# Kernel optimization log

Hardware: AMD Instinct MI355X
Metric: run time of the kernel (lower is better)

Reference implementation:

```python
import jax, jax.numpy as jnp
import numpy as np

N = 50000       # nodes
E = 800000      # edges (avg degree 16)
IN_DIM = 128
EDGE_DIM = 32
OUT_DIM = 128


def setup_inputs() -> dict:
    key = jax.random.key(0)
    ks = jax.random.split(key, 7)
    nfeat = jax.random.normal(ks[0], (N, IN_DIM), jnp.float32)
    etype = jax.random.normal(ks[1], (E, EDGE_DIM), jnp.float32)
    src = jax.random.randint(ks[2], (E,), 0, N)
    dst = jax.random.randint(ks[3], (E,), 0, N)
    scaled = lambda k, shape, fan: jax.random.normal(k, shape, jnp.float32) / np.sqrt(fan).astype(np.float32)
    W_edge = scaled(ks[4], (OUT_DIM, EDGE_DIM), EDGE_DIM)          # edge_map.weight
    W_ne = scaled(ks[5], (OUT_DIM, IN_DIM + OUT_DIM), IN_DIM + OUT_DIM)  # fc_neigh_edge.weight
    b_ne = jnp.zeros((OUT_DIM,), jnp.float32)
    W_self = scaled(ks[6], (OUT_DIM, IN_DIM), IN_DIM)              # fc_self.weight
    b_self = jnp.zeros((OUT_DIM,), jnp.float32)
    eps = jnp.zeros((1,), jnp.float32)                             # init_eps = 0, not learned
    return dict(nfeat=nfeat, etype=etype, src=src, dst=dst,
                W_edge=W_edge, W_ne=W_ne, b_ne=b_ne,
                W_self=W_self, b_self=b_self, eps=eps)


def reference(nfeat, etype, src, dst, W_edge, W_ne, b_ne, W_self, b_self, eps):
    # per-edge message: relu(fc_neigh_edge(cat(src_h, edge_map(etype))))
    # split W_ne to avoid materializing the concatenated [E, in+out] tensor
    W1 = W_ne[:, :IN_DIM]    # acts on src node features
    W2 = W_ne[:, IN_DIM:]    # acts on mapped edge features
    eh = etype @ W_edge.T                              # [E, out]
    src_h = nfeat[src]                                 # gather [E, in]
    m = jax.nn.relu(src_h @ W1.T + eh @ W2.T + b_ne)   # [E, out]
    # max-reduce messages to destination nodes (DGL max reducer; 0 for isolated nodes)
    neigh = jax.ops.segment_max(m, dst, num_segments=N)
    deg = jax.ops.segment_sum(jnp.ones((E,), m.dtype), dst, num_segments=N)
    neigh = jnp.where((deg > 0)[:, None], neigh, jnp.zeros((), m.dtype))
    out = (1.0 + eps) * neigh + (nfeat @ W_self.T + b_self)
    return out
```

## Files before the change

kernel.cpp:

```cpp
#include <hip/hip_runtime.h>
#include <hip/hip_bf16.h>

#define NNODES 50000
#define NEDGES 800000
#define IN_DIM 128
#define EDGE_DIM 32
#define OUT_DIM 128
#define KDIM 160
#define A_STRIDE 168
#define NS 136
#define MT_STRIDE 72
#define NT (NEDGES / 64)
#define EG 768

typedef __attribute__((ext_vector_type(8))) short short8;
typedef __attribute__((ext_vector_type(4))) short short4v;
typedef __attribute__((ext_vector_type(4))) float floatx4;

__device__ __forceinline__ short f2bf(float f) {
    union { float f; unsigned u; } v; v.f = f;
    unsigned r = (v.u + 0x7FFFu + ((v.u >> 16) & 1u)) >> 16;
    return (short)r;
}

__device__ __forceinline__ void store_bf4(short* p, floatx4 v) {
    short4v s;
    s.x = f2bf(v.x); s.y = f2bf(v.y); s.z = f2bf(v.z); s.w = f2bf(v.w);
    *(short4v*)p = s;
}

__device__ __forceinline__ void store_bf8(short* p, floatx4 a, floatx4 b) {
    short8 s;
    s[0] = f2bf(a.x); s[1] = f2bf(a.y); s[2] = f2bf(a.z); s[3] = f2bf(a.w);
    s[4] = f2bf(b.x); s[5] = f2bf(b.y); s[6] = f2bf(b.z); s[7] = f2bf(b.w);
    *(short8*)p = s;
}

#define MFMA8(ACC, A0, A1, B0, B1, B2, B3)                                        \
    ACC[0][0] = __builtin_amdgcn_mfma_f32_16x16x32_bf16(A0, B0, ACC[0][0], 0, 0, 0); \
    ACC[0][1] = __builtin_amdgcn_mfma_f32_16x16x32_bf16(A0, B1, ACC[0][1], 0, 0, 0); \
    ACC[0][2] = __builtin_amdgcn_mfma_f32_16x16x32_bf16(A0, B2, ACC[0][2], 0, 0, 0); \
    ACC[0][3] = __builtin_amdgcn_mfma_f32_16x16x32_bf16(A0, B3, ACC[0][3], 0, 0, 0); \
    ACC[1][0] = __builtin_amdgcn_mfma_f32_16x16x32_bf16(A1, B0, ACC[1][0], 0, 0, 0); \
    ACC[1][1] = __builtin_amdgcn_mfma_f32_16x16x32_bf16(A1, B1, ACC[1][1], 0, 0, 0); \
    ACC[1][2] = __builtin_amdgcn_mfma_f32_16x16x32_bf16(A1, B2, ACC[1][2], 0, 0, 0); \
    ACC[1][3] = __builtin_amdgcn_mfma_f32_16x16x32_bf16(A1, B3, ACC[1][3], 0, 0, 0);

__global__ __launch_bounds__(256) void prep_kernel(
    const float* __restrict__ nfeat, const int* __restrict__ dst,
    const float* __restrict__ W_edge, const float* __restrict__ W_ne,
    const float* __restrict__ W_self, float* __restrict__ out,
    int* __restrict__ cnt, short* __restrict__ nfB,
    short* __restrict__ WcatB, short* __restrict__ WselfB)
{
    int gid = blockIdx.x * 256 + threadIdx.x;
    int GS = gridDim.x * 256;
    for (int i = gid; i < NNODES * OUT_DIM / 4; i += GS)
        ((floatx4*)out)[i] = (floatx4){0.f, 0.f, 0.f, 0.f};
    for (int i = gid; i < NNODES * IN_DIM / 8; i += GS) {
        floatx4 a = ((const floatx4*)nfeat)[2 * i];
        floatx4 b = ((const floatx4*)nfeat)[2 * i + 1];
        store_bf8(nfB + 8 * i, a, b);
    }
    for (int idx = gid; idx < OUT_DIM * KDIM + OUT_DIM * IN_DIM; idx += GS) {
        if (idx < OUT_DIM * KDIM) {
            int n = idx / KDIM, k = idx - n * KDIM;
            float val;
            if (k < IN_DIM) {
                val = W_ne[n * 256 + k];
            } else {
                int j = k - IN_DIM;
                float s = 0.f;
                for (int kk = 0; kk < 128; ++kk)
                    s += W_ne[n * 256 + 128 + kk] * W_edge[kk * 32 + j];
                val = s;
            }
            WcatB[idx] = f2bf(val);
        } else {
            int s = idx - OUT_DIM * KDIM;
            WselfB[s] = f2bf(W_self[s]);
        }
    }
    for (int e = gid; e < NEDGES; e += GS)
        atomicAdd(&cnt[dst[e]], 1);
}

__global__ __launch_bounds__(1024) void scan_kernel(const int* __restrict__ cnt,
                                                    int* __restrict__ cur) {
    __shared__ int bufA[1024], bufB[1024];
    const int CH = 49;
    int t = threadIdx.x;
    int beg = t * CH, end = min(beg + CH, NNODES);
    int s = 0;
    for (int i = beg; i < end; ++i) s += cnt[i];
    bufA[t] = s;
    __syncthreads();
    int* in = bufA; int* out = bufB;
    for (int off = 1; off < 1024; off <<= 1) {
        out[t] = in[t] + (t >= off ? in[t - off] : 0);
        __syncthreads();
        int* tmp = in; in = out; out = tmp;
    }
    int base = in[t] - s;
    for (int i = beg; i < end; ++i) { cur[i] = base; base += cnt[i]; }
}

__global__ void scatter_kernel(const int* __restrict__ src,
                               const int* __restrict__ dst,
                               int* __restrict__ cur,
                               int2* __restrict__ epack) {
    int e = blockIdx.x * 256 + threadIdx.x;
    if (e < NEDGES) {
        int d = dst[e];
        int s = src[e];
        int pos = atomicAdd(&cur[d], 1);
        int2 r;
        r.x = (int)((unsigned)s | ((unsigned)d << 16));
        r.y = e;
        epack[pos] = r;
    }
}

__global__ __launch_bounds__(256, 3) void edge_kernel(
    const short* __restrict__ nfB, const float* __restrict__ etype,
    const int2* __restrict__ epack, const float* __restrict__ b_ne,
    const short* __restrict__ WcatB, float* __restrict__ out)
{
    __shared__ short As[64 * A_STRIDE];
    __shared__ unsigned short mT[128 * MT_STRIDE];

    const int tid = threadIdx.x;
    const int lane = tid & 63;
    const int w = tid >> 6;
    const int li = lane & 15, q = lane >> 4;

    short8 bf[2][5];
    #pragma unroll
    for (int ct = 0; ct < 2; ++ct)
        #pragma unroll
        for (int kk = 0; kk < 5; ++kk)
            bf[ct][kk] = *(const short8*)(WcatB +
                (size_t)(w * 32 + ct * 16 + li) * KDIM + kk * 32 + q * 8);

    float bias[2];
    #pragma unroll
    for (int ct = 0; ct < 2; ++ct) bias[ct] = b_ne[w * 32 + ct * 16 + li];

    const int ee = tid >> 2, ec = tid & 3;

    short8 pv0, pv1, pv2, pv3;
    floatx4 pf0, pf1;
    int2 pnext; pnext.x = 0; pnext.y = 0;

    const int tA = blockIdx.x;

    {
        int2 pc = epack[tA * 64 + ee];
        int s = pc.x & 0xFFFF;
        const short8* nr = (const short8*)(nfB + (size_t)s * 128);
        pv0 = nr[4 * ec]; pv1 = nr[4 * ec + 1];
        pv2 = nr[4 * ec + 2]; pv3 = nr[4 * ec + 3];
        const floatx4* er = (const floatx4*)(etype + (size_t)pc.y * 32);
        pf0 = er[2 * ec]; pf1 = er[2 * ec + 1];

        int tB = tA + EG;
        int2 pcB; pcB.x = 0; pcB.y = 0;
        if (tB < NT) pcB = epack[tB * 64 + ee];

        short* ap = As + ee * A_STRIDE + 32 * ec;
        *(short8*)(ap)      = pv0;
        *(short8*)(ap + 8)  = pv1;
        *(short8*)(ap + 16) = pv2;
        *(short8*)(ap + 24) = pv3;
        store_bf8(As + ee * A_STRIDE + IN_DIM + 8 * ec, pf0, pf1);

        if (tB < NT) {
            int sB = pcB.x & 0xFFFF;
            const short8* nrB = (const short8*)(nfB + (size_t)sB * 128);
            pv0 = nrB[4 * ec]; pv1 = nrB[4 * ec + 1];
            pv2 = nrB[4 * ec + 2]; pv3 = nrB[4 * ec + 3];
            const floatx4* erB = (const floatx4*)(etype + (size_t)pcB.y * 32);
            pf0 = erB[2 * ec]; pf1 = erB[2 * ec + 1];
            int tC = tB + EG;
            if (tC < NT) pnext = epack[tC * 64 + ee];
        }
    }

    for (int t = tA; t < NT; t += EG) {
        const int e0 = t * 64;

        asm volatile("s_waitcnt lgkmcnt(0)" ::: "memory");
        __builtin_amdgcn_s_barrier();

        floatx4 acc[4][2];
        #pragma unroll
        for (int i = 0; i < 4; ++i)
            #pragma unroll
            for (int j = 0; j < 2; ++j)
                acc[i][j] = (floatx4){0.f, 0.f, 0.f, 0.f};

        #pragma unroll
        for (int kk = 0; kk < 5; ++kk) {
            short8 a0 = *(const short8*)(As + (0 * 16 + li) * A_STRIDE + kk * 32 + q * 8);
            short8 a1 = *(const short8*)(As + (1 * 16 + li) * A_STRIDE + kk * 32 + q * 8);
            short8 a2 = *(const short8*)(As + (2 * 16 + li) * A_STRIDE + kk * 32 + q * 8);
            short8 a3 = *(const short8*)(As + (3 * 16 + li) * A_STRIDE + kk * 32 + q * 8);
            acc[0][0] = __builtin_amdgcn_mfma_f32_16x16x32_bf16(a0, bf[0][kk], acc[0][0], 0, 0, 0);
            acc[0][1] = __builtin_amdgcn_mfma_f32_16x16x32_bf16(a0, bf[1][kk], acc[0][1], 0, 0, 0);
            acc[1][0] = __builtin_amdgcn_mfma_f32_16x16x32_bf16(a1, bf[0][kk], acc[1][0], 0, 0, 0);
            acc[1][1] = __builtin_amdgcn_mfma_f32_16x16x32_bf16(a1, bf[1][kk], acc[1][1], 0, 0, 0);
            acc[2][0] = __builtin_amdgcn_mfma_f32_16x16x32_bf16(a2, bf[0][kk], acc[2][0], 0, 0, 0);
            acc[2][1] = __builtin_amdgcn_mfma_f32_16x16x32_bf16(a2, bf[1][kk], acc[2][1], 0, 0, 0);
            acc[3][0] = __builtin_amdgcn_mfma_f32_16x16x32_bf16(a3, bf[0][kk], acc[3][0], 0, 0, 0);
            acc[3][1] = __builtin_amdgcn_mfma_f32_16x16x32_bf16(a3, bf[1][kk], acc[3][1], 0, 0, 0);
        }

        #pragma unroll
        for (int rt = 0; rt < 4; ++rt) {
            #pragma unroll
            for (int ct = 0; ct < 2; ++ct) {
                floatx4 a = acc[rt][ct];
                short4v s;
                float v0 = a.x + bias[ct]; s.x = f2bf(v0 > 0.f ? v0 : 0.f);
                float v1 = a.y + bias[ct]; s.y = f2bf(v1 > 0.f ? v1 : 0.f);
                float v2 = a.z + bias[ct]; s.z = f2bf(v2 > 0.f ? v2 : 0.f);
                float v3 = a.w + bias[ct]; s.w = f2bf(v3 > 0.f ? v3 : 0.f);
                *(short4v*)((short*)mT + (w * 32 + ct * 16 + li) * MT_STRIDE
                            + rt * 16 + q * 4) = s;
            }
        }
        asm volatile("s_waitcnt lgkmcnt(0)" ::: "memory");
        __builtin_amdgcn_s_barrier();

        {
            int tn = t + EG;
            if (tn < NT) {
                short* ap = As + ee * A_STRIDE + 32 * ec;
                *(short8*)(ap)      = pv0;
                *(short8*)(ap + 8)  = pv1;
                *(short8*)(ap + 16) = pv2;
                *(short8*)(ap + 24) = pv3;
                store_bf8(As + ee * A_STRIDE + IN_DIM + 8 * ec, pf0, pf1);

                int2 pc2 = pnext;
                int t2 = tn + EG;
                if (t2 < NT) {
                    int t3 = t2 + EG;
                    if (t3 < NT) pnext = epack[t3 * 64 + ee];
                    int s2 = pc2.x & 0xFFFF;
                    const short8* nr2 = (const short8*)(nfB + (size_t)s2 * 128);
                    pv0 = nr2[4 * ec]; pv1 = nr2[4 * ec + 1];
                    pv2 = nr2[4 * ec + 2]; pv3 = nr2[4 * ec + 3];
                    const floatx4* er2 = (const floatx4*)(etype + (size_t)pc2.y * 32);
                    pf0 = er2[2 * ec]; pf1 = er2[2 * ec + 1];
                }
            }
        }
        __builtin_amdgcn_sched_barrier(0);

        {
            int c = tid & 127, h = tid >> 7;
            int r0 = h * 32;
            const int4* dp = (const int4*)(epack + (e0 + r0));
            int dd[32];
            #pragma unroll
            for (int i = 0; i < 16; ++i) {
                int4 v = dp[i];
                dd[2 * i]     = (int)((unsigned)v.x >> 16);
                dd[2 * i + 1] = (int)((unsigned)v.z >> 16);
            }
            unsigned mval[32];
            #pragma unroll
            for (int j = 0; j < 4; ++j) {
                short8 v = *(const short8*)((const short*)mT + c * MT_STRIDE
                                            + r0 + 8 * j);
                #pragma unroll
                for (int k = 0; k < 8; ++k)
                    mval[8 * j + k] = (unsigned short)v[k];
            }
            int curd = dd[0];
            unsigned best = mval[0];
            #pragma unroll
            for (int r = 1; r < 32; ++r) {
                if (dd[r] != curd) {
                    atomicMax((int*)out + (size_t)curd * 128 + c,
                              (int)(best << 16));
                    curd = dd[r]; best = mval[r];
                } else {
                    best = best > mval[r] ? best : mval[r];
                }
            }
            atomicMax((int*)out + (size_t)curd * 128 + c, (int)(best << 16));
        }
    }
}

__global__ __launch_bounds__(256) void node_kernel(
    const short* __restrict__ nfB, const float* __restrict__ b_self,
    const float* __restrict__ eps, const short* __restrict__ WselfB,
    float* __restrict__ out)
{
    __shared__ short As[64 * NS];
    __shared__ short Bs[128 * NS];
    const int tid = threadIdx.x;
    const int n0 = blockIdx.x * 64;

    {
        int r = tid >> 1, h = tid & 1;
        const short8* g = (const short8*)(WselfB + r * 128 + h * 64);
        short* l = Bs + r * NS + h * 64;
        #pragma unroll
        for (int c = 0; c < 8; ++c)
            *(short8*)(l + 8 * c) = g[c];
    }
    {
        int r = tid >> 2, c = tid & 3;
        int n = n0 + r;
        short* ap = As + r * NS + 32 * c;
        if (n < NNODES) {
            const short8* nr = (const short8*)(nfB + (size_t)n * 128);
            #pragma unroll
            for (int j = 0; j < 4; ++j)
                *(short8*)(ap + 8 * j) = nr[4 * c + j];
        } else {
            #pragma unroll
            for (int j = 0; j < 4; ++j)
                *(short8*)(ap + 8 * j) = (short8){0,0,0,0,0,0,0,0};
        }
    }
    __syncthreads();

    const int lane = tid & 63;
    const int w = tid >> 6;
    const int et = w & 1;
    const int nh = w >> 1;
    const int li = lane & 15, q = lane >> 4;

    floatx4 acc[2][4];
    #pragma unroll
    for (int i = 0; i < 2; ++i)
        #pragma unroll
        for (int j = 0; j < 4; ++j)
            acc[i][j] = (floatx4){0.f, 0.f, 0.f, 0.f};

    const short* Ab = As + (et * 32 + li) * NS + q * 8;
    const short* Bb = Bs + (nh * 64 + li) * NS + q * 8;
    #pragma unroll
    for (int kk = 0; kk < 4; ++kk) {
        short8 a0 = *(const short8*)(Ab + kk * 32);
        short8 a1 = *(const short8*)(Ab + 16 * NS + kk * 32);
        short8 b0 = *(const short8*)(Bb + kk * 32);
        short8 b1 = *(const short8*)(Bb + 16 * NS + kk * 32);
        short8 b2 = *(const short8*)(Bb + 32 * NS + kk * 32);
        short8 b3 = *(const short8*)(Bb + 48 * NS + kk * 32);
        MFMA8(acc, a0, a1, b0, b1, b2, b3)
    }

    const float epsv = 1.0f + eps[0];
    #pragma unroll
    for (int ta = 0; ta < 2; ++ta) {
        #pragma unroll
        for (int r = 0; r < 4; ++r) {
            int n = n0 + et * 32 + ta * 16 + q * 4 + r;
            if (n < NNODES) {
                #pragma unroll
                for (int tb = 0; tb < 4; ++tb) {
                    int o = nh * 64 + tb * 16 + li;
                    float v = acc[ta][tb][r] + b_self[o]
                            + epsv * out[(size_t)n * 128 + o];
                    out[(size_t)n * 128 + o] = v;
                }
            }
        }
    }
}

__global__ void prep_w(const float* __restrict__ W_edge,
                       const float* __restrict__ W_ne,
                       const float* __restrict__ W_self,
                       short* __restrict__ WcatB, short* __restrict__ WselfB)
{
    int idx = blockIdx.x * 256 + threadIdx.x;
    if (idx < OUT_DIM * KDIM) {
        int n = idx / KDIM, k = idx - n * KDIM;
        float val;
        if (k < IN_DIM) {
            val = W_ne[n * 256 + k];
        } else {
            int j = k - IN_DIM;
            float s = 0.f;
            for (int kk = 0; kk < 128; ++kk)
                s += W_ne[n * 256 + 128 + kk] * W_edge[kk * 32 + j];
            val = s;
        }
        WcatB[idx] = f2bf(val);
    } else if (idx < OUT_DIM * KDIM + OUT_DIM * IN_DIM) {
        int s = idx - OUT_DIM * KDIM;
        WselfB[s] = f2bf(W_self[s]);
    }
}

__global__ __launch_bounds__(256) void edge_direct(
    const float* __restrict__ nfeat, const float* __restrict__ etype,
    const int* __restrict__ src, const int* __restrict__ dst,
    const float* __restrict__ b_ne, const short* __restrict__ WcatB,
    float* __restrict__ out)
{
    __shared__ short As[64 * A_STRIDE];
    __shared__ short Bs[128 * A_STRIDE];
    const int tid = threadIdx.x;
    const int e0 = blockIdx.x * 64;
    {
        int r = tid >> 1, h = tid & 1;
        const short8* g = (const short8*)(WcatB + r * KDIM + h * 80);
        short* l = Bs + r * A_STRIDE + h * 80;
        #pragma unroll
        for (int c = 0; c < 10; ++c) *(short8*)(l + 8 * c) = g[c];
    }
    {
        const floatx4* ge = (const floatx4*)(etype + (size_t)e0 * 32);
        #pragma unroll
        for (int i = 0; i < 2; ++i) {
            int f = tid + i * 256;
            int e = f >> 3, c = f & 7;
            store_bf4(As + e * A_STRIDE + IN_DIM + 4 * c, ge[f]);
        }
    }
    {
        int g = tid & 15, eo = tid >> 4;
        #pragma unroll
        for (int p = 0; p < 4; ++p) {
            int e = eo + p * 16;
            int s = src[e0 + e];
            const floatx4* row = (const floatx4*)(nfeat + (size_t)s * 128);
            floatx4 v0 = row[g];
            floatx4 v1 = row[g + 16];
            store_bf4(As + e * A_STRIDE + 4 * g, v0);
            store_bf4(As + e * A_STRIDE + 64 + 4 * g, v1);
        }
    }
    __syncthreads();
    const int lane = tid & 63;
    const int w = tid >> 6;
    const int et = w & 1, nh = w >> 1;
    const int li = lane & 15, q = lane >> 4;
    floatx4 acc[2][4];
    #pragma unroll
    for (int i = 0; i < 2; ++i)
        #pragma unroll
        for (int j = 0; j < 4; ++j)
            acc[i][j] = (floatx4){0.f, 0.f, 0.f, 0.f};
    const short* Ab = As + (et * 32 + li) * A_STRIDE + q * 8;
    const short* Bb = Bs + (nh * 64 + li) * A_STRIDE + q * 8;
    #pragma unroll
    for (int kk = 0; kk < 5; ++kk) {
        short8 a0 = *(const short8*)(Ab + kk * 32);
        short8 a1 = *(const short8*)(Ab + 16 * A_STRIDE + kk * 32);
        short8 b0 = *(const short8*)(Bb + kk * 32);
        short8 b1 = *(const short8*)(Bb + 16 * A_STRIDE + kk * 32);
        short8 b2 = *(const short8*)(Bb + 32 * A_STRIDE + kk * 32);
        short8 b3 = *(const short8*)(Bb + 48 * A_STRIDE + kk * 32);
        MFMA8(acc, a0, a1, b0, b1, b2, b3)
    }
    #pragma unroll
    for (int ta = 0; ta < 2; ++ta) {
        #pragma unroll
        for (int r = 0; r < 4; ++r) {
            int el = et * 32 + ta * 16 + q * 4 + r;
            int d = dst[e0 + el];
            int* nrow = (int*)out + (size_t)d * 128;
            #pragma unroll
            for (int tb = 0; tb < 4; ++tb) {
                int o = nh * 64 + tb * 16 + li;
                float v = acc[ta][tb][r] + b_ne[o];
                v = v > 0.f ? v : 0.f;
                atomicMax(nrow + o, __float_as_int(v));
            }
        }
    }
}

__global__ __launch_bounds__(256) void node_direct(
    const float* __restrict__ nfeat, const float* __restrict__ b_self,
    const float* __restrict__ eps, const short* __restrict__ WselfB,
    float* __restrict__ out)
{
    __shared__ short As[64 * NS];
    __shared__ short Bs[128 * NS];
    const int tid = threadIdx.x;
    const int n0 = blockIdx.x * 64;
    {
        int r = tid >> 1, h = tid & 1;
        const short8* g = (const short8*)(WselfB + r * 128 + h * 64);
        short* l = Bs + r * NS + h * 64;
        #pragma unroll
        for (int c = 0; c < 8; ++c) *(short8*)(l + 8 * c) = g[c];
    }
    {
        int r = tid >> 2, fi = tid & 3;
        int n = n0 + r;
        if (n < NNODES) {
            const floatx4* row = (const floatx4*)(nfeat + (size_t)n * 128);
            #pragma unroll
            for (int p = 0; p < 8; ++p) {
                int f = fi + 4 * p;
                store_bf4(As + r * NS + 4 * f, row[f]);
            }
        } else {
            #pragma unroll
            for (int p = 0; p < 8; ++p) {
                int f = fi + 4 * p;
                *(short4v*)(As + r * NS + 4 * f) = (short4v){0, 0, 0, 0};
            }
        }
    }
    __syncthreads();
    const int lane = tid & 63;
    const int w = tid >> 6;
    const int et = w & 1, nh = w >> 1;
    const int li = lane & 15, q = lane >> 4;
    floatx4 acc[2][4];
    #pragma unroll
    for (int i = 0; i < 2; ++i)
        #pragma unroll
        for (int j = 0; j < 4; ++j)
            acc[i][j] = (floatx4){0.f, 0.f, 0.f, 0.f};
    const short* Ab = As + (et * 32 + li) * NS + q * 8;
    const short* Bb = Bs + (nh * 64 + li) * NS + q * 8;
    #pragma unroll
    for (int kk = 0; kk < 4; ++kk) {
        short8 a0 = *(const short8*)(Ab + kk * 32);
        short8 a1 = *(const short8*)(Ab + 16 * NS + kk * 32);
        short8 b0 = *(const short8*)(Bb + kk * 32);
        short8 b1 = *(const short8*)(Bb + 16 * NS + kk * 32);
        short8 b2 = *(const short8*)(Bb + 32 * NS + kk * 32);
        short8 b3 = *(const short8*)(Bb + 48 * NS + kk * 32);
        MFMA8(acc, a0, a1, b0, b1, b2, b3)
    }
    const float epsv = 1.0f + eps[0];
    #pragma unroll
    for (int ta = 0; ta < 2; ++ta) {
        #pragma unroll
        for (int r = 0; r < 4; ++r) {
            int n = n0 + et * 32 + ta * 16 + q * 4 + r;
            if (n < NNODES) {
                #pragma unroll
                for (int tb = 0; tb < 4; ++tb) {
                    int o = nh * 64 + tb * 16 + li;
                    float v = acc[ta][tb][r] + b_self[o]
                            + epsv * out[(size_t)n * 128 + o];
                    out[(size_t)n * 128 + o] = v;
                }
            }
        }
    }
}

extern "C" void kernel_launch(void* const* d_in, const int* in_sizes, int n_in,
                              void* d_out, int out_size, void* d_ws, size_t ws_size,
                              hipStream_t stream) {
    const float* nfeat  = (const float*)d_in[0];
    const float* etype  = (const float*)d_in[1];
    const int*   src    = (const int*)d_in[2];
    const int*   dst    = (const int*)d_in[3];
    const float* W_edge = (const float*)d_in[4];
    const float* W_ne   = (const float*)d_in[5];
    const float* b_ne   = (const float*)d_in[6];
    const float* W_self = (const float*)d_in[7];
    const float* b_self = (const float*)d_in[8];
    const float* eps    = (const float*)d_in[9];
    float* out = (float*)d_out;

    char* ws = (char*)d_ws;
    size_t off = 0;
    auto alloc = [&](size_t bytes) { void* p = ws + off; off = (off + bytes + 255) & ~(size_t)255; return p; };
    int*   cnt    = (int*)alloc((size_t)NNODES * 4);
    int*   cur    = (int*)alloc((size_t)NNODES * 4);
    int2*  epack  = (int2*)alloc((size_t)NEDGES * 8);
    short* nfB    = (short*)alloc((size_t)NNODES * IN_DIM * 2);
    short* WcatB  = (short*)alloc((size_t)OUT_DIM * KDIM * 2);
    short* WselfB = (short*)alloc((size_t)OUT_DIM * IN_DIM * 2);
    size_t need = off;

    if (ws_size >= need) {
        hipMemsetAsync(cnt, 0, (size_t)NNODES * 4, stream);
        prep_kernel<<<1024, 256, 0, stream>>>(nfeat, dst, W_edge, W_ne, W_self,
                                              out, cnt, nfB, WcatB, WselfB);
        scan_kernel<<<1, 1024, 0, stream>>>(cnt, cur);
        scatter_kernel<<<(NEDGES + 255) / 256, 256, 0, stream>>>(
            src, dst, cur, epack);
        edge_kernel<<<EG, 256, 0, stream>>>(nfB, etype, epack, b_ne, WcatB, out);
        node_kernel<<<(NNODES + 63) / 64, 256, 0, stream>>>(nfB, b_self, eps,
                                                            WselfB, out);
    } else {
        short* WcatB2  = (short*)d_ws;
        short* WselfB2 = WcatB2 + (size_t)OUT_DIM * KDIM;
        hipMemsetAsync(out, 0, (size_t)NNODES * 128 * sizeof(float), stream);
        prep_w<<<144, 256, 0, stream>>>(W_edge, W_ne, W_self, WcatB2, WselfB2);
        edge_direct<<<NEDGES / 64, 256, 0, stream>>>(nfeat, etype, src, dst,
                                                     b_ne, WcatB2, out);
        node_direct<<<(NNODES + 63) / 64, 256, 0, stream>>>(nfeat, b_self, eps,
                                                            WselfB2, out);
    }
}
```

Before: 431.9 us.

## Stage destination ids in LDS, raise occupancy and grid, prioritize MFMA

Destination ids for each tile are now written into a double-buffered LDS array during the A-tile staging step. Each thread reads 32 of them and makes them wave-uniform with readfirstlane, instead of reloading 32 packed edge records from global memory per thread. This frees the dd[32] register array, which lets launch bounds go from 3 to 4 waves per SIMD and the persistent grid from 768 to 1024 blocks. The MFMA loop also runs at raised wave priority. More resident blocks means more LDS and register pressure per CU.

Result: no change. 437.8 us (+1.4%).

```diff
diff --git a/kernel.cpp b/kernel.cpp
--- a/kernel.cpp
+++ b/kernel.cpp
@@ -11,7 +11,7 @@
 #define NS 136
 #define MT_STRIDE 72
 #define NT (NEDGES / 64)
-#define EG 768
+#define EG 1024
 
 typedef __attribute__((ext_vector_type(8))) short short8;
 typedef __attribute__((ext_vector_type(4))) short short4v;
@@ -121,13 +121,14 @@
     }
 }
 
-__global__ __launch_bounds__(256, 3) void edge_kernel(
+__global__ __launch_bounds__(256, 4) void edge_kernel(
     const short* __restrict__ nfB, const float* __restrict__ etype,
     const int2* __restrict__ epack, const float* __restrict__ b_ne,
     const short* __restrict__ WcatB, float* __restrict__ out)
 {
     __shared__ short As[64 * A_STRIDE];
     __shared__ unsigned short mT[128 * MT_STRIDE];
+    __shared__ short dstL[2][64];
 
     const int tid = threadIdx.x;
     const int lane = tid & 63;
@@ -150,6 +151,7 @@
 
     short8 pv0, pv1, pv2, pv3;
     floatx4 pf0, pf1;
+    int2 rcur; rcur.x = 0; rcur.y = 0;
     int2 pnext; pnext.x = 0; pnext.y = 0;
 
     const int tA = blockIdx.x;
@@ -173,6 +175,7 @@
         *(short8*)(ap + 16) = pv2;
         *(short8*)(ap + 24) = pv3;
         store_bf8(As + ee * A_STRIDE + IN_DIM + 8 * ec, pf0, pf1);
+        if (ec == 0) dstL[0][ee] = (short)((unsigned)pc.x >> 16);
 
         if (tB < NT) {
             int sB = pcB.x & 0xFFFF;
@@ -181,13 +184,15 @@
             pv2 = nrB[4 * ec + 2]; pv3 = nrB[4 * ec + 3];
             const floatx4* erB = (const floatx4*)(etype + (size_t)pcB.y * 32);
             pf0 = erB[2 * ec]; pf1 = erB[2 * ec + 1];
+            rcur = pcB;
             int tC = tB + EG;
             if (tC < NT) pnext = epack[tC * 64 + ee];
         }
     }
 
-    for (int t = tA; t < NT; t += EG) {
-        const int e0 = t * 64;
+    int it = 0;
+    for (int t = tA; t < NT; t += EG, ++it) {
+        const int cb = it & 1, nb = cb ^ 1;
 
         asm volatile("s_waitcnt lgkmcnt(0)" ::: "memory");
         __builtin_amdgcn_s_barrier();
@@ -199,6 +204,7 @@
             for (int j = 0; j < 2; ++j)
                 acc[i][j] = (floatx4){0.f, 0.f, 0.f, 0.f};
 
+        __builtin_amdgcn_s_setprio(1);
         #pragma unroll
         for (int kk = 0; kk < 5; ++kk) {
             short8 a0 = *(const short8*)(As + (0 * 16 + li) * A_STRIDE + kk * 32 + q * 8);
@@ -214,6 +220,7 @@
             acc[3][0] = __builtin_amdgcn_mfma_f32_16x16x32_bf16(a3, bf[0][kk], acc[3][0], 0, 0, 0);
             acc[3][1] = __builtin_amdgcn_mfma_f32_16x16x32_bf16(a3, bf[1][kk], acc[3][1], 0, 0, 0);
         }
+        __builtin_amdgcn_s_setprio(0);
 
         #pragma unroll
         for (int rt = 0; rt < 4; ++rt) {
@@ -241,6 +248,7 @@
                 *(short8*)(ap + 16) = pv2;
                 *(short8*)(ap + 24) = pv3;
                 store_bf8(As + ee * A_STRIDE + IN_DIM + 8 * ec, pf0, pf1);
+                if (ec == 0) dstL[nb][ee] = (short)((unsigned)rcur.x >> 16);
 
                 int2 pc2 = pnext;
                 int t2 = tn + EG;
@@ -253,6 +261,7 @@
                     pv2 = nr2[4 * ec + 2]; pv3 = nr2[4 * ec + 3];
                     const floatx4* er2 = (const floatx4*)(etype + (size_t)pc2.y * 32);
                     pf0 = er2[2 * ec]; pf1 = er2[2 * ec + 1];
+                    rcur = pc2;
                 }
             }
         }
@@ -261,14 +270,6 @@
         {
             int c = tid & 127, h = tid >> 7;
             int r0 = h * 32;
-            const int4* dp = (const int4*)(epack + (e0 + r0));
-            int dd[32];
-            #pragma unroll
-            for (int i = 0; i < 16; ++i) {
-                int4 v = dp[i];
-                dd[2 * i]     = (int)((unsigned)v.x >> 16);
-                dd[2 * i + 1] = (int)((unsigned)v.z >> 16);
-            }
             unsigned mval[32];
             #pragma unroll
             for (int j = 0; j < 4; ++j) {
@@ -278,16 +279,26 @@
                 for (int k = 0; k < 8; ++k)
                     mval[8 * j + k] = (unsigned short)v[k];
             }
-            int curd = dd[0];
-            unsigned best = mval[0];
-            #pragma unroll
-            for (int r = 1; r < 32; ++r) {
-                if (dd[r] != curd) {
-                    atomicMax((int*)out + (size_t)curd * 128 + c,
-                              (int)(best << 16));
-                    curd = dd[r]; best = mval[r];
-                } else {
-                    best = best > mval[r] ? best : mval[r];
+            const short8* dls = (const short8*)(&dstL[cb][r0]);
+            int curd = 0;
+            unsigned best = 0;
+            #pragma unroll
+            for (int j = 0; j < 4; ++j) {
+                short8 dv = dls[j];
+                #pragma unroll
+                for (int k = 0; k < 8; ++k) {
+                    int r = 8 * j + k;
+                    int d = __builtin_amdgcn_readfirstlane(
+                        (int)(unsigned short)dv[k]);
+                    if (r == 0) {
+                        curd = d; best = mval[0];
+                    } else if (d != curd) {
+                        atomicMax((int*)out + (size_t)curd * 128 + c,
+                                  (int)(best << 16));
+                        curd = d; best = mval[r];
+                    } else {
+                        best = best > mval[r] ? best : mval[r];
+                    }
                 }
             }
             atomicMax((int*)out + (size_t)curd * 128 + c, (int)(best << 16));
```
